# Kernel optimization log

Hardware: AMD Instinct MI355X
Metric: run time of the kernel (lower is better)

Reference implementation:

```python
import jax, jax.numpy as jnp
import numpy as np

HID = 10


def _lstm_cell(xt, h, c, W_ih, W_hh, b_ih, b_hh):
    # PyTorch LSTMCell: gates ordered (i, f, g, o)
    gates = xt @ W_ih.T + b_ih + h @ W_hh.T + b_hh  # [B, 4*HID]
    i, f, g, o = jnp.split(gates, 4, axis=-1)
    c_new = jax.nn.sigmoid(f) * c + jax.nn.sigmoid(i) * jnp.tanh(g)
    h_new = jax.nn.sigmoid(o) * jnp.tanh(c_new)
    return h_new, c_new


def setup_inputs() -> dict:
    key = jax.random.key(0)
    ks = jax.random.split(key, 12)
    B, T = 2048, 1024
    s = 0.1
    return {
        "x": jax.random.normal(ks[0], (B, T), dtype=jnp.float32),
        "W_ih1": jax.random.normal(ks[1], (4 * HID, 1), dtype=jnp.float32) * s,
        "W_hh1": jax.random.normal(ks[2], (4 * HID, HID), dtype=jnp.float32) * s,
        "b_ih1": jax.random.normal(ks[3], (4 * HID,), dtype=jnp.float32) * s,
        "b_hh1": jax.random.normal(ks[4], (4 * HID,), dtype=jnp.float32) * s,
        "W_ih2": jax.random.normal(ks[5], (4 * HID, HID), dtype=jnp.float32) * s,
        "W_hh2": jax.random.normal(ks[6], (4 * HID, HID), dtype=jnp.float32) * s,
        "b_ih2": jax.random.normal(ks[7], (4 * HID,), dtype=jnp.float32) * s,
        "b_ih2b": None,  # placeholder removed below
        "b_hh2": jax.random.normal(ks[8], (4 * HID,), dtype=jnp.float32) * s,
        "W_lin": jax.random.normal(ks[9], (1, HID), dtype=jnp.float32) * s,
        "b_lin": jax.random.normal(ks[10], (1,), dtype=jnp.float32) * s,
        "future": 64,
    } if False else {
        "x": jax.random.normal(ks[0], (B, T), dtype=jnp.float32),
        "W_ih1": jax.random.normal(ks[1], (4 * HID, 1), dtype=jnp.float32) * s,
        "W_hh1": jax.random.normal(ks[2], (4 * HID, HID), dtype=jnp.float32) * s,
        "b_ih1": jax.random.normal(ks[3], (4 * HID,), dtype=jnp.float32) * s,
        "b_hh1": jax.random.normal(ks[4], (4 * HID,), dtype=jnp.float32) * s,
        "W_ih2": jax.random.normal(ks[5], (4 * HID, HID), dtype=jnp.float32) * s,
        "W_hh2": jax.random.normal(ks[6], (4 * HID, HID), dtype=jnp.float32) * s,
        "b_ih2": jax.random.normal(ks[7], (4 * HID,), dtype=jnp.float32) * s,
        "b_hh2": jax.random.normal(ks[8], (4 * HID,), dtype=jnp.float32) * s,
        "W_lin": jax.random.normal(ks[9], (1, HID), dtype=jnp.float32) * s,
        "b_lin": jax.random.normal(ks[10], (1,), dtype=jnp.float32) * s,
        "future": 64,
    }


def _forward(x, W_ih1, W_hh1, b_ih1, b_hh1, W_ih2, W_hh2, b_ih2, b_hh2,
             W_lin, b_lin, future):
    B = x.shape[0]
    z = jnp.zeros((B, HID), dtype=x.dtype)
    state0 = (z, z, z, z)  # h1, c1, h2, c2

    def step(state, xt):
        h1, c1, h2, c2 = state
        h1, c1 = _lstm_cell(xt, h1, c1, W_ih1, W_hh1, b_ih1, b_hh1)
        h2, c2 = _lstm_cell(h1, h2, c2, W_ih2, W_hh2, b_ih2, b_hh2)
        y = h2 @ W_lin.T + b_lin  # [B, 1]
        return (h1, c1, h2, c2), y

    xs = x.T[:, :, None]  # [T, B, 1]
    state, ys = jax.lax.scan(step, state0, xs)  # ys: [T, B, 1]
    outs = ys[:, :, 0].T  # [B, T]

    if future > 0:
        last = ys[-1]  # [B, 1]

        def fstep(carry, _):
            state, y = carry
            state, y_new = step(state, y)
            return (state, y_new), y_new

        (_, _), fys = jax.lax.scan(fstep, (state, last), None, length=future)
        outs = jnp.concatenate([outs, fys[:, :, 0].T], axis=1)
    return outs  # [B, T + future]


def reference(x, W_ih1, W_hh1, b_ih1, b_hh1, W_ih2, W_hh2, b_ih2, b_hh2,
              W_lin, b_lin, future):
    return _forward(x, W_ih1, W_hh1, b_ih1, b_hh1, W_ih2, W_hh2, b_ih2,
                    b_hh2, W_lin, b_lin, future)
```

## Files before the change

### kernel.cpp

```cpp
#include <hip/hip_runtime.h>


#define NB 512
#define TMAIN 1024
#define HID 10
#define KCH 16
#define NCH (TMAIN / KCH)

typedef float v2f __attribute__((ext_vector_type(2)));
typedef float v4f __attribute__((ext_vector_type(4)));

#define PIN2(v) asm volatile("" : "+v"(v))
#define PIN(v)  asm volatile("" : "+v"(v))

__device__ __forceinline__ float rcp_(float v)  { return __builtin_amdgcn_rcpf(v); }
__device__ __forceinline__ float exp2_(float v) { return __builtin_amdgcn_exp2f(v); }
__device__ __forceinline__ v2f mk2(float x, float y) { v2f r; r.x = x; r.y = y; return r; }
__device__ __forceinline__ v2f pfma2(v2f a, v2f b, v2f c) { return __builtin_elementwise_fma(a, b, c); }

template<int J>
__device__ __forceinline__ float bc16(float v) {
    return __int_as_float(__builtin_amdgcn_ds_swizzle(__float_as_int(v), (J << 5) | 0x10));
}
__device__ __forceinline__ void bcast10(float h, float* hb) {
    hb[0] = bc16<0>(h); hb[1] = bc16<1>(h); hb[2] = bc16<2>(h); hb[3] = bc16<3>(h);
    hb[4] = bc16<4>(h); hb[5] = bc16<5>(h); hb[6] = bc16<6>(h); hb[7] = bc16<7>(h);
    hb[8] = bc16<8>(h); hb[9] = bc16<9>(h);
}

__global__ __launch_bounds__(256)
void lstm2_kernel(
    const float* __restrict__ x,
    const float* __restrict__ Wih1, const float* __restrict__ Whh1,
    const float* __restrict__ bih1, const float* __restrict__ bhh1,
    const float* __restrict__ Wih2, const float* __restrict__ Whh2,
    const float* __restrict__ bih2, const float* __restrict__ bhh2,
    const float* __restrict__ Wlin, const float* __restrict__ blin,
    const int* __restrict__ futp,
    float* __restrict__ out)
{
    const int tid  = threadIdx.x;
    const int wid  = tid >> 6;
    const int lane = tid & 63;
    const int e    = lane >> 4;
    const int u    = lane & 15;
    const int ge   = blockIdx.x * 4 + e;
    const int F    = futp[0];
    const int OUTW = TMAIN + F;

    __shared__ __align__(16) float ringH1[2][KCH][64];
    __shared__ __align__(16) v4f   ringU [2][KCH][64];
    __shared__ __align__(16) float ringH2[2][KCH][64];
    __shared__ __align__(16) float stC1[64], stH1[64], stC2[64], stH2[64];

    const bool uok = (u < HID);
    const int  uu  = uok ? u : 0;
    const int  Ri  = 0 * HID + uu;
    const int  Rf  = 1 * HID + uu;
    const int  Rg  = 2 * HID + uu;
    const int  Ro  = 3 * HID + uu;

    const float tK = 2.8853900817779268f;
    const float sK = -1.4426950408889634f;
    const float mu = uok ? 1.f : 0.f;
    const float sKm = mu * sK;
    const float tKm = mu * tK;

    v2f w1_if[10], w1_go[10], w2i_if[10], w2i_go[10], w2h_if[10], w2h_go[10];
    v2f wlp[5];
    #pragma unroll
    for (int j = 0; j < HID; ++j) {
        w1_if[j]  = mk2(sKm * Whh1[Ri*HID + j], sKm * Whh1[Rf*HID + j]);
        w1_go[j]  = mk2(tKm * Whh1[Rg*HID + j], sKm * Whh1[Ro*HID + j]);
        w2i_if[j] = mk2(sKm * Wih2[Ri*HID + j], sKm * Wih2[Rf*HID + j]);
        w2i_go[j] = mk2(tKm * Wih2[Rg*HID + j], sKm * Wih2[Ro*HID + j]);
        w2h_if[j] = mk2(sKm * Whh2[Ri*HID + j], sKm * Whh2[Rf*HID + j]);
        w2h_go[j] = mk2(tKm * Whh2[Rg*HID + j], sKm * Whh2[Ro*HID + j]);
    }
    #pragma unroll
    for (int k = 0; k < 5; ++k) wlp[k] = mk2(Wlin[2*k], Wlin[2*k + 1]);
    v2f b1_if = mk2(sKm * (bih1[Ri] + bhh1[Ri]), sKm * (bih1[Rf] + bhh1[Rf]));
    v2f b1_go = mk2(tKm * (bih1[Rg] + bhh1[Rg]), sKm * (bih1[Ro] + bhh1[Ro]));
    v2f b2_if = mk2(sKm * (bih2[Ri] + bhh2[Ri]), sKm * (bih2[Rf] + bhh2[Rf]));
    v2f b2_go = mk2(tKm * (bih2[Rg] + bhh2[Rg]), sKm * (bih2[Ro] + bhh2[Ro]));
    v2f wx_if = mk2(sKm * Wih1[Ri], sKm * Wih1[Rf]);
    v2f wx_go = mk2(tKm * Wih1[Rg], sKm * Wih1[Ro]);
    float bl = blin[0];

    #pragma unroll
    for (int j = 0; j < HID; ++j) {
        PIN2(w1_if[j]); PIN2(w1_go[j]); PIN2(w2i_if[j]); PIN2(w2i_go[j]);
        PIN2(w2h_if[j]); PIN2(w2h_go[j]);
    }
    #pragma unroll
    for (int k = 0; k < 5; ++k) PIN2(wlp[k]);
    PIN2(b1_if); PIN2(b1_go); PIN2(b2_if); PIN2(b2_go); PIN2(wx_if); PIN2(wx_go); PIN(bl);

    auto ctanh_ = [&](float cs) -> float {
        return fmaf(-2.0f, rcp_(1.0f + exp2_(cs)), 1.0f);
    };
    auto cellup2 = [&](v2f p_if, v2f p_go, float& c) -> float {
        v2f q_if, q_go;
        q_if.x = rcp_(1.0f + exp2_(p_if.x));
        q_if.y = rcp_(1.0f + exp2_(p_if.y));
        q_go.x = rcp_(1.0f + exp2_(p_go.x));
        q_go.y = rcp_(1.0f + exp2_(p_go.y));
        float g = fmaf(-2.0f * tK, q_go.x, tK);
        c = fmaf(q_if.y, c, q_if.x * g);
        return q_go.y * ctanh_(c);
    };
    auto dotp = [&](const v2f* w, const float* hb, v2f init) -> v2f {
        v2f P = pfma2(w[0], mk2(hb[0], hb[0]), init);
        v2f Q = w[1] * mk2(hb[1], hb[1]);
        #pragma unroll
        for (int j = 2; j < HID; j += 2) {
            P = pfma2(w[j],     mk2(hb[j],     hb[j]),     P);
            Q = pfma2(w[j + 1], mk2(hb[j + 1], hb[j + 1]), Q);
        }
        return P + Q;
    };
    auto loadhb = [&](const float* base, float* hb) {
        v4f a = *(const v4f*)(base);
        v4f b = *(const v4f*)(base + 4);
        v2f c = *(const v2f*)(base + 8);
        hb[0] = a.x; hb[1] = a.y; hb[2] = a.z; hb[3] = a.w;
        hb[4] = b.x; hb[5] = b.y; hb[6] = b.z; hb[7] = b.w;
        hb[8] = c.x; hb[9] = c.y;
    };

    float c1 = 0.f, c2 = 0.f, h1last = 0.f, h2last = 0.f, yprev = 0.f;
    float h1b[10], h2b[10];
    #pragma unroll
    for (int j = 0; j < HID; ++j) { h1b[j] = 0.f; h2b[j] = 0.f; }

    auto head_ = [&]() -> float {
        v2f Y = pfma2(wlp[0], mk2(h2b[0], h2b[1]), mk2(bl, 0.f));
        #pragma unroll
        for (int k = 1; k < 5; ++k)
            Y = pfma2(wlp[k], mk2(h2b[2*k], h2b[2*k + 1]), Y);
        return Y.x + Y.y;
    };

    auto pstep0 = [&](float xt, float* hslot) -> float {
        v2f A_if = dotp(w1_if, h1b, pfma2(wx_if, mk2(xt, xt), b1_if));
        v2f A_go = dotp(w1_go, h1b, pfma2(wx_go, mk2(xt, xt), b1_go));
        float h1n = cellup2(A_if, A_go, c1);
        bcast10(h1n, h1b);
        hslot[lane] = h1n;
        return h1n;
    };
    auto fstep = [&](float yt) -> float {
        v2f A_if = dotp(w1_if, h1b, pfma2(wx_if, mk2(yt, yt), b1_if));
        v2f A_go = dotp(w1_go, h1b, pfma2(wx_go, mk2(yt, yt), b1_go));
        float h1n = cellup2(A_if, A_go, c1);
        bcast10(h1n, h1b);
        v2f U_if = dotp(w2i_if, h1b, b2_if);
        v2f U_go = dotp(w2i_go, h1b, b2_go);
        v2f V_if = dotp(w2h_if, h2b, mk2(U_if.x, U_if.y));
        v2f V_go = dotp(w2h_go, h2b, mk2(U_go.x, U_go.y));
        float h2n = cellup2(V_if, V_go, c2);
        bcast10(h2n, h2b);
        return head_();
    };

    const float4* xrow = (const float4*)(x + (size_t)ge * TMAIN);
    float4* orow = (float4*)(out + (size_t)ge * OUTW);

    float4 z4 = make_float4(0.f, 0.f, 0.f, 0.f);
    float4 xq0 = z4, xq1 = z4, xq2 = z4, xq3 = z4;
    if (wid == 0) { xq0 = xrow[0]; xq1 = xrow[1]; xq2 = xrow[2]; xq3 = xrow[3]; }

    #pragma unroll 1
    for (int c = 0; c <= NCH + 2; ++c) {
        if (wid == 0) {
            if (c < NCH) {
                float4 xn0 = z4, xn1 = z4, xn2 = z4, xn3 = z4;
                if (c + 1 < NCH) {
                    xn0 = xrow[(c+1)*4+0]; xn1 = xrow[(c+1)*4+1];
                    xn2 = xrow[(c+1)*4+2]; xn3 = xrow[(c+1)*4+3];
                }
                float* hs = &ringH1[c & 1][0][0];
                h1last = pstep0(xq0.x, hs + 0*64);  h1last = pstep0(xq0.y, hs + 1*64);
                h1last = pstep0(xq0.z, hs + 2*64);  h1last = pstep0(xq0.w, hs + 3*64);
                h1last = pstep0(xq1.x, hs + 4*64);  h1last = pstep0(xq1.y, hs + 5*64);
                h1last = pstep0(xq1.z, hs + 6*64);  h1last = pstep0(xq1.w, hs + 7*64);
                h1last = pstep0(xq2.x, hs + 8*64);  h1last = pstep0(xq2.y, hs + 9*64);
                h1last = pstep0(xq2.z, hs + 10*64); h1last = pstep0(xq2.w, hs + 11*64);
                h1last = pstep0(xq3.x, hs + 12*64); h1last = pstep0(xq3.y, hs + 13*64);
                h1last = pstep0(xq3.z, hs + 14*64); h1last = pstep0(xq3.w, hs + 15*64);
                if (c == NCH - 1) { stC1[lane] = c1; stH1[lane] = h1last; }
                xq0 = xn0; xq1 = xn1; xq2 = xn2; xq3 = xn3;
            }
        } else if (wid == 1) {
            const int cc = c - 1;
            if (cc >= 0 && cc < NCH) {
                const float* hs = &ringH1[cc & 1][0][0];
                v4f* us = &ringU[cc & 1][0][0];
                #pragma unroll
                for (int t = 0; t < KCH; ++t) {
                    float hb[10];
                    loadhb(hs + t*64 + e*16, hb);
                    v2f U_if = dotp(w2i_if, hb, b2_if);
                    v2f U_go = dotp(w2i_go, hb, b2_go);
                    v4f U; U.x = U_if.x; U.y = U_if.y; U.z = U_go.x; U.w = U_go.y;
                    us[t*64 + lane] = U;
                }
            }
        } else if (wid == 2) {
            const int cc = c - 2;
            if (cc >= 0 && cc < NCH) {
                const v4f* us = &ringU[cc & 1][0][0];
                float* h2s = &ringH2[cc & 1][0][0];
                #pragma unroll
                for (int t = 0; t < KCH; ++t) {
                    v4f U = us[t*64 + lane];
                    v2f V_if = dotp(w2h_if, h2b, mk2(U.x, U.y));
                    v2f V_go = dotp(w2h_go, h2b, mk2(U.z, U.w));
                    float h2n = cellup2(V_if, V_go, c2);
                    bcast10(h2n, h2b);
                    h2s[t*64 + lane] = h2n;
                    h2last = h2n;
                }
                if (cc == NCH - 1) { stC2[lane] = c2; stH2[lane] = h2last; }
            }
        } else {
            const int cc = c - 3;
            if (cc >= 0 && cc < NCH) {
                const float* h2s = &ringH2[cc & 1][0][0];
                #pragma unroll
                for (int q = 0; q < 4; ++q) {
                    float y0, y1, y2, y3;
                    loadhb(h2s + (q*4 + 0)*64 + e*16, h2b); y0 = head_();
                    loadhb(h2s + (q*4 + 1)*64 + e*16, h2b); y1 = head_();
                    loadhb(h2s + (q*4 + 2)*64 + e*16, h2b); y2 = head_();
                    loadhb(h2s + (q*4 + 3)*64 + e*16, h2b); y3 = head_();
                    if (u == 0) orow[cc*4 + q] = make_float4(y0, y1, y2, y3);
                    yprev = y3;
                }
            }
        }
        __syncthreads();
    }

    if (wid == 3) {
        c1 = stC1[lane];
        c2 = stC2[lane];
        loadhb(&stH1[e*16], h1b);
        loadhb(&stH2[e*16], h2b);
        float yp = yprev;
        int t = 0;
        #pragma unroll 1
        for (; t + 3 < F; t += 4) {
            float y0 = fstep(yp);
            float y1 = fstep(y0);
            float y2 = fstep(y1);
            float y3 = fstep(y2);
            if (u == 0) orow[(TMAIN + t) / 4] = make_float4(y0, y1, y2, y3);
            yp = y3;
        }
        #pragma unroll 1
        for (; t < F; ++t) {
            yp = fstep(yp);
            if (u == 0) out[(size_t)ge * OUTW + TMAIN + t] = yp;
        }
    }
}

extern "C" void kernel_launch(void* const* d_in, const int* in_sizes, int n_in,
                              void* d_out, int out_size, void* d_ws, size_t ws_size,
                              hipStream_t stream) {
    const float* x    = (const float*)d_in[0];
    const float* Wih1 = (const float*)d_in[1];
    const float* Whh1 = (const float*)d_in[2];
    const float* bih1 = (const float*)d_in[3];
    const float* bhh1 = (const float*)d_in[4];
    const float* Wih2 = (const float*)d_in[5];
    const float* Whh2 = (const float*)d_in[6];
    const float* bih2 = (const float*)d_in[7];
    const float* bhh2 = (const float*)d_in[8];
    const float* Wlin = (const float*)d_in[9];
    const float* blin = (const float*)d_in[10];
    const int*   futp = (const int*)d_in[11];
    float* out = (float*)d_out;

    lstm2_kernel<<<NB, 256, 0, stream>>>(x, Wih1, Whh1, bih1, bhh1,
                                         Wih2, Whh2, bih2, bhh2,
                                         Wlin, blin, futp, out);
}
```

Measured before the change: 324.2 us.

## Replace ds_swizzle broadcast with DPP row-rotate and rotated weight layout

The recurrent matvecs in the layer-1 and layer-2 recurrence warps now take the hidden state through DPP row_ror rotations instead of ten ds_swizzle broadcasts. Weights are pre-permuted per lane into a 16-entry rotated layout, with the rotation direction detected at runtime. This avoids the LDS-path swizzle latency on the serial critical path, at the cost of 16 FMAs instead of 10 per dot product. Weight loading is also split by warp role to cut register pressure, and the future-step weights are loaded only in the last warp.

```diff
diff --git a/kernel.cpp b/kernel.cpp
--- a/kernel.cpp
+++ b/kernel.cpp
@@ -18,6 +18,19 @@
 __device__ __forceinline__ v2f mk2(float x, float y) { v2f r; r.x = x; r.y = y; return r; }
 __device__ __forceinline__ v2f pfma2(v2f a, v2f b, v2f c) { return __builtin_elementwise_fma(a, b, c); }
 
+template<int R>
+__device__ __forceinline__ float rorf(float v) {
+    return __int_as_float(__builtin_amdgcn_update_dpp(
+        0, __float_as_int(v), 0x120 + R, 0xF, 0xF, true));
+}
+__device__ __forceinline__ void rot16(float h, float* hr) {
+    hr[0] = h;
+    hr[1]  = rorf<1>(h);  hr[2]  = rorf<2>(h);  hr[3]  = rorf<3>(h);
+    hr[4]  = rorf<4>(h);  hr[5]  = rorf<5>(h);  hr[6]  = rorf<6>(h);
+    hr[7]  = rorf<7>(h);  hr[8]  = rorf<8>(h);  hr[9]  = rorf<9>(h);
+    hr[10] = rorf<10>(h); hr[11] = rorf<11>(h); hr[12] = rorf<12>(h);
+    hr[13] = rorf<13>(h); hr[14] = rorf<14>(h); hr[15] = rorf<15>(h);
+}
 template<int J>
 __device__ __forceinline__ float bc16(float v) {
     return __int_as_float(__builtin_amdgcn_ds_swizzle(__float_as_int(v), (J << 5) | 0x10));
@@ -66,35 +79,52 @@
     const float sKm = mu * sK;
     const float tKm = mu * tK;
 
-    v2f w1_if[10], w1_go[10], w2i_if[10], w2i_go[10], w2h_if[10], w2h_go[10];
+    const int rot1 = __builtin_amdgcn_update_dpp(0, u, 0x121, 0xF, 0xF, true);
+    const bool dplus = (rot1 == ((u + 1) & 15));
+
+    v2f wrot_if[16], wrot_go[16];
+    v2f w2i_if[10], w2i_go[10];
     v2f wlp[5];
-    #pragma unroll
-    for (int j = 0; j < HID; ++j) {
-        w1_if[j]  = mk2(sKm * Whh1[Ri*HID + j], sKm * Whh1[Rf*HID + j]);
-        w1_go[j]  = mk2(tKm * Whh1[Rg*HID + j], sKm * Whh1[Ro*HID + j]);
-        w2i_if[j] = mk2(sKm * Wih2[Ri*HID + j], sKm * Wih2[Rf*HID + j]);
-        w2i_go[j] = mk2(tKm * Wih2[Rg*HID + j], sKm * Wih2[Ro*HID + j]);
-        w2h_if[j] = mk2(sKm * Whh2[Ri*HID + j], sKm * Whh2[Rf*HID + j]);
-        w2h_go[j] = mk2(tKm * Whh2[Rg*HID + j], sKm * Whh2[Ro*HID + j]);
-    }
-    #pragma unroll
-    for (int k = 0; k < 5; ++k) wlp[k] = mk2(Wlin[2*k], Wlin[2*k + 1]);
-    v2f b1_if = mk2(sKm * (bih1[Ri] + bhh1[Ri]), sKm * (bih1[Rf] + bhh1[Rf]));
-    v2f b1_go = mk2(tKm * (bih1[Rg] + bhh1[Rg]), sKm * (bih1[Ro] + bhh1[Ro]));
-    v2f b2_if = mk2(sKm * (bih2[Ri] + bhh2[Ri]), sKm * (bih2[Rf] + bhh2[Rf]));
-    v2f b2_go = mk2(tKm * (bih2[Rg] + bhh2[Rg]), sKm * (bih2[Ro] + bhh2[Ro]));
-    v2f wx_if = mk2(sKm * Wih1[Ri], sKm * Wih1[Rf]);
-    v2f wx_go = mk2(tKm * Wih1[Rg], sKm * Wih1[Ro]);
+    v2f wx_if = mk2(0.f, 0.f), wx_go = wx_if;
+    v2f b1_if = wx_if, b1_go = wx_if, b2_if = wx_if, b2_go = wx_if;
     float bl = blin[0];
 
-    #pragma unroll
-    for (int j = 0; j < HID; ++j) {
-        PIN2(w1_if[j]); PIN2(w1_go[j]); PIN2(w2i_if[j]); PIN2(w2i_go[j]);
-        PIN2(w2h_if[j]); PIN2(w2h_go[j]);
-    }
-    #pragma unroll
-    for (int k = 0; k < 5; ++k) PIN2(wlp[k]);
-    PIN2(b1_if); PIN2(b1_go); PIN2(b2_if); PIN2(b2_go); PIN2(wx_if); PIN2(wx_go); PIN(bl);
+    if (wid == 0 || wid == 2) {
+        const float* W = (wid == 0) ? Whh1 : Whh2;
+        #pragma unroll
+        for (int r = 0; r < 16; ++r) {
+            int jr = (u + (dplus ? r : 16 - r)) & 15;
+            int jc = (jr < HID) ? jr : 0;
+            float m = (uok && jr < HID) ? 1.f : 0.f;
+            wrot_if[r] = mk2(m * sK * W[Ri*HID + jc], m * sK * W[Rf*HID + jc]);
+            wrot_go[r] = mk2(m * tK * W[Rg*HID + jc], m * sK * W[Ro*HID + jc]);
+        }
+        #pragma unroll
+        for (int r = 0; r < 16; ++r) { PIN2(wrot_if[r]); PIN2(wrot_go[r]); }
+    }
+    if (wid == 0) {
+        wx_if = mk2(sKm * Wih1[Ri], sKm * Wih1[Rf]);
+        wx_go = mk2(tKm * Wih1[Rg], sKm * Wih1[Ro]);
+        b1_if = mk2(sKm * (bih1[Ri] + bhh1[Ri]), sKm * (bih1[Rf] + bhh1[Rf]));
+        b1_go = mk2(tKm * (bih1[Rg] + bhh1[Rg]), sKm * (bih1[Ro] + bhh1[Ro]));
+        PIN2(wx_if); PIN2(wx_go); PIN2(b1_if); PIN2(b1_go);
+    }
+    if (wid == 1) {
+        #pragma unroll
+        for (int j = 0; j < HID; ++j) {
+            w2i_if[j] = mk2(sKm * Wih2[Ri*HID + j], sKm * Wih2[Rf*HID + j]);
+            w2i_go[j] = mk2(tKm * Wih2[Rg*HID + j], sKm * Wih2[Ro*HID + j]);
+        }
+        b2_if = mk2(sKm * (bih2[Ri] + bhh2[Ri]), sKm * (bih2[Rf] + bhh2[Rf]));
+        b2_go = mk2(tKm * (bih2[Rg] + bhh2[Rg]), sKm * (bih2[Ro] + bhh2[Ro]));
+        #pragma unroll
+        for (int j = 0; j < HID; ++j) { PIN2(w2i_if[j]); PIN2(w2i_go[j]); }
+        PIN2(b2_if); PIN2(b2_go);
+    }
+    if (wid == 3) {
+        #pragma unroll
+        for (int k = 0; k < 5; ++k) { wlp[k] = mk2(Wlin[2*k], Wlin[2*k + 1]); PIN2(wlp[k]); }
+    }
 
     auto ctanh_ = [&](float cs) -> float {
         return fmaf(-2.0f, rcp_(1.0f + exp2_(cs)), 1.0f);
@@ -119,6 +149,16 @@
         }
         return P + Q;
     };
+    auto dot16rot = [&](const v2f* w, const float* hr, v2f init) -> v2f {
+        v2f P = pfma2(w[0], mk2(hr[0], hr[0]), init);
+        v2f Q = w[1] * mk2(hr[1], hr[1]);
+        #pragma unroll
+        for (int r = 2; r < 16; r += 2) {
+            P = pfma2(w[r],     mk2(hr[r],     hr[r]),     P);
+            Q = pfma2(w[r + 1], mk2(hr[r + 1], hr[r + 1]), Q);
+        }
+        return P + Q;
+    };
     auto loadhb = [&](const float* base, float* hb) {
         v4f a = *(const v4f*)(base);
         v4f b = *(const v4f*)(base + 4);
@@ -129,9 +169,12 @@
     };
 
     float c1 = 0.f, c2 = 0.f, h1last = 0.f, h2last = 0.f, yprev = 0.f;
-    float h1b[10], h2b[10];
+    float h1r[16], h2r[16];
+    float h2b[10];
     #pragma unroll
-    for (int j = 0; j < HID; ++j) { h1b[j] = 0.f; h2b[j] = 0.f; }
+    for (int r = 0; r < 16; ++r) { h1r[r] = 0.f; h2r[r] = 0.f; }
+    #pragma unroll
+    for (int j = 0; j < HID; ++j) h2b[j] = 0.f;
 
     auto head_ = [&]() -> float {
         v2f Y = pfma2(wlp[0], mk2(h2b[0], h2b[1]), mk2(bl, 0.f));
@@ -142,25 +185,12 @@
     };
 
     auto pstep0 = [&](float xt, float* hslot) -> float {
-        v2f A_if = dotp(w1_if, h1b, pfma2(wx_if, mk2(xt, xt), b1_if));
-        v2f A_go = dotp(w1_go, h1b, pfma2(wx_go, mk2(xt, xt), b1_go));
+        v2f A_if = dot16rot(wrot_if, h1r, pfma2(wx_if, mk2(xt, xt), b1_if));
+        v2f A_go = dot16rot(wrot_go, h1r, pfma2(wx_go, mk2(xt, xt), b1_go));
         float h1n = cellup2(A_if, A_go, c1);
-        bcast10(h1n, h1b);
+        rot16(h1n, h1r);
         hslot[lane] = h1n;
         return h1n;
-    };
-    auto fstep = [&](float yt) -> float {
-        v2f A_if = dotp(w1_if, h1b, pfma2(wx_if, mk2(yt, yt), b1_if));
-        v2f A_go = dotp(w1_go, h1b, pfma2(wx_go, mk2(yt, yt), b1_go));
-        float h1n = cellup2(A_if, A_go, c1);
-        bcast10(h1n, h1b);
-        v2f U_if = dotp(w2i_if, h1b, b2_if);
-        v2f U_go = dotp(w2i_go, h1b, b2_go);
-        v2f V_if = dotp(w2h_if, h2b, mk2(U_if.x, U_if.y));
-        v2f V_go = dotp(w2h_go, h2b, mk2(U_go.x, U_go.y));
-        float h2n = cellup2(V_if, V_go, c2);
-        bcast10(h2n, h2b);
-        return head_();
     };
 
     const float4* xrow = (const float4*)(x + (size_t)ge * TMAIN);
@@ -214,10 +244,10 @@
                 #pragma unroll
                 for (int t = 0; t < KCH; ++t) {
                     v4f U = us[t*64 + lane];
-                    v2f V_if = dotp(w2h_if, h2b, mk2(U.x, U.y));
-                    v2f V_go = dotp(w2h_go, h2b, mk2(U.z, U.w));
+                    v2f V_if = dot16rot(wrot_if, h2r, mk2(U.x, U.y));
+                    v2f V_go = dot16rot(wrot_go, h2r, mk2(U.z, U.w));
                     float h2n = cellup2(V_if, V_go, c2);
-                    bcast10(h2n, h2b);
+                    rot16(h2n, h2r);
                     h2s[t*64 + lane] = h2n;
                     h2last = h2n;
                 }
@@ -243,10 +273,43 @@
     }
 
     if (wid == 3) {
+        v2f f1_if[10], f1_go[10], f2i_if[10], f2i_go[10], f2h_if[10], f2h_go[10];
+        #pragma unroll
+        for (int j = 0; j < HID; ++j) {
+            f1_if[j]  = mk2(sKm * Whh1[Ri*HID + j], sKm * Whh1[Rf*HID + j]);
+            f1_go[j]  = mk2(tKm * Whh1[Rg*HID + j], sKm * Whh1[Ro*HID + j]);
+            f2i_if[j] = mk2(sKm * Wih2[Ri*HID + j], sKm * Wih2[Rf*HID + j]);
+            f2i_go[j] = mk2(tKm * Wih2[Rg*HID + j], sKm * Wih2[Ro*HID + j]);
+            f2h_if[j] = mk2(sKm * Whh2[Ri*HID + j], sKm * Whh2[Rf*HID + j]);
+            f2h_go[j] = mk2(tKm * Whh2[Rg*HID + j], sKm * Whh2[Ro*HID + j]);
+        }
+        v2f fb1_if = mk2(sKm * (bih1[Ri] + bhh1[Ri]), sKm * (bih1[Rf] + bhh1[Rf]));
+        v2f fb1_go = mk2(tKm * (bih1[Rg] + bhh1[Rg]), sKm * (bih1[Ro] + bhh1[Ro]));
+        v2f fb2_if = mk2(sKm * (bih2[Ri] + bhh2[Ri]), sKm * (bih2[Rf] + bhh2[Rf]));
+        v2f fb2_go = mk2(tKm * (bih2[Rg] + bhh2[Rg]), sKm * (bih2[Ro] + bhh2[Ro]));
+        v2f fwx_if = mk2(sKm * Wih1[Ri], sKm * Wih1[Rf]);
+        v2f fwx_go = mk2(tKm * Wih1[Rg], sKm * Wih1[Ro]);
+
+        float h1b[10];
         c1 = stC1[lane];
         c2 = stC2[lane];
         loadhb(&stH1[e*16], h1b);
         loadhb(&stH2[e*16], h2b);
+
+        auto fstep = [&](float yt) -> float {
+            v2f A_if = dotp(f1_if, h1b, pfma2(fwx_if, mk2(yt, yt), fb1_if));
+            v2f A_go = dotp(f1_go, h1b, pfma2(fwx_go, mk2(yt, yt), fb1_go));
+            float h1n = cellup2(A_if, A_go, c1);
+            bcast10(h1n, h1b);
+            v2f U_if = dotp(f2i_if, h1b, fb2_if);
+            v2f U_go = dotp(f2i_go, h1b, fb2_go);
+            v2f V_if = dotp(f2h_if, h2b, mk2(U_if.x, U_if.y));
+            v2f V_go = dotp(f2h_go, h2b, mk2(U_go.x, U_go.y));
+            float h2n = cellup2(V_if, V_go, c2);
+            bcast10(h2n, h2b);
+            return head_();
+        };
+
         float yp = yprev;
         int t = 0;
         #pragma unroll 1
```

Result: slower. 381.2 us (+17.6%).
